# Optimization experiments

Measured on AMD Instinct MI355X. Metric: run time of the kernel, lower is better.

The kernel has to match this reference:

```python
import jax, jax.numpy as jnp
import numpy as np

D_MODEL = 1024
N_HEAD = 16
D_HEAD = 64
BSZ = 2
QLEN = 2048
LOCAL_SIZE = 1000
LN_EPS = 1e-5


def setup_inputs() -> dict:
    key = jax.random.key(0)
    ks = jax.random.split(key, 8)
    z1ss = jax.random.normal(ks[0], (BSZ, D_MODEL, QLEN), jnp.float32)
    pos_emb = jax.random.normal(ks[1], (1, D_MODEL, QLEN), jnp.float32)
    u1ss = jax.random.normal(ks[2], (BSZ, 3 * N_HEAD * D_HEAD, QLEN), jnp.float32) * 0.05
    W_qkv = jax.random.normal(ks[3], (3 * N_HEAD * D_HEAD, D_MODEL), jnp.float32) * 0.02
    W_r = jax.random.normal(ks[4], (N_HEAD * D_HEAD, D_MODEL), jnp.float32) * 0.02
    r_w_bias = jax.random.uniform(ks[5], (N_HEAD, D_HEAD), jnp.float32, -0.05, 0.05)
    r_r_bias = jax.random.uniform(ks[6], (N_HEAD, D_HEAD), jnp.float32, -0.05, 0.05)
    W_o = jax.random.normal(ks[7], (D_MODEL, N_HEAD * D_HEAD), jnp.float32) * 0.02
    b_o = jnp.zeros((D_MODEL,), jnp.float32)
    return dict(z1ss=z1ss, pos_emb=pos_emb, u1ss=u1ss, W_qkv=W_qkv, W_r=W_r,
                r_w_bias=r_w_bias, r_r_bias=r_r_bias, W_o=W_o, b_o=b_o)


def _rel_shift(x):
    # Transformer-XL relative-shift trick: pad one column on the left, reshape,
    # drop first row, reshape back. x: [b, n, qlen, klen]
    b, n, q, k = x.shape
    xp = jnp.pad(x, ((0, 0), (0, 0), (0, 0), (1, 0)))
    return xp.reshape(b, n, k + 1, q)[:, :, 1:, :].reshape(b, n, q, k)


def reference(z1ss, pos_emb, u1ss, W_qkv, W_r, r_w_bias, r_r_bias, W_o, b_o):
    bsz, d_model, qlen = z1ss.shape
    n_head, d_head = r_w_bias.shape
    klen = qlen  # mems=None -> mlen=0
    scale = 1.0 / (d_head ** 0.5)

    # Conv1d(kernel_size=1, bias=False) == per-position linear
    w_heads = jnp.einsum('od,bdq->boq', W_qkv, z1ss) + u1ss        # [b, 3*n*d, q]
    r_head_k = jnp.einsum('od,dq->oq', W_r, pos_emb[0]).reshape(n_head, d_head, klen)

    q_h, k_h, v_h = jnp.split(w_heads, 3, axis=1)
    q_h = q_h.reshape(bsz, n_head, d_head, qlen)
    k_h = k_h.reshape(bsz, n_head, d_head, klen)
    v_h = v_h.reshape(bsz, n_head, d_head, klen)

    AC = jnp.einsum('bndi,bndj->bnij', q_h + r_w_bias[:, :, None], k_h)
    BD = _rel_shift(jnp.einsum('bndi,ndj->bnij', q_h + r_r_bias[:, :, None], r_head_k))
    attn_score = (AC + BD) * scale                                  # [b, n, q, k]

    # causal + local-window mask (mlen=0)
    ones = jnp.ones((qlen, klen), dtype=bool)
    mask = jnp.triu(ones, 1) | jnp.tril(ones, -LOCAL_SIZE)
    attn_score = jnp.where(mask[None, None], -jnp.inf, attn_score)

    attn_prob = jax.nn.softmax(attn_score, axis=-1)
    attn_vec = jnp.einsum('bnij,bndj->bndi', attn_prob, v_h)
    attn_vec = attn_vec.reshape(bsz, n_head * d_head, qlen)

    attn_out = jnp.einsum('od,bdq->boq', W_o, attn_vec) + b_o[None, :, None]

    # post-LN residual: layer_norm over d_model (no affine params)
    x = (attn_out + z1ss).transpose(0, 2, 1)                        # [b, q, d]
    mu = x.mean(-1, keepdims=True)
    var = ((x - mu) ** 2).mean(-1, keepdims=True)
    x = (x - mu) / jnp.sqrt(var + LN_EPS)
    return x.transpose(0, 2, 1)                                     # [b, d, q]
```

## Files before the change

### kernel.cpp

```cpp
#include <hip/hip_runtime.h>
#include <hip/hip_bf16.h>

#define D_MODEL 1024
#define N_HEAD 16
#define BSZ 2
#define QLEN 2048
#define LOCAL_SIZE 1000
#define QKV3 (3 * N_HEAD * 64)

typedef __hip_bfloat16 bf16;
typedef short bf16x8 __attribute__((ext_vector_type(8)));
typedef float f32x4 __attribute__((ext_vector_type(4)));

static __device__ __forceinline__ float b2f(bf16 x) { return __bfloat162float(x); }
static __device__ __forceinline__ float bits2f(unsigned short u) {
    return __uint_as_float(((unsigned int)u) << 16);
}
static __device__ __forceinline__ unsigned short f2bs(float x) {
    __hip_bfloat16 h = __float2bfloat16(x);
    return *(unsigned short*)&h;
}

static __device__ __forceinline__ int rmode(int m, int fl) { return (m == 2) ? fl : m; }
static __device__ __forceinline__ float ldm(const void* p, size_t i, int isf) {
    return isf ? ((const float*)p)[i] : b2f(((const bf16*)p)[i]);
}
static __device__ __forceinline__ float4 ld4(const void* p, size_t i, int isf) {
    if (isf) return ((const float4*)p)[i >> 2];
    ushort4 u = ((const ushort4*)p)[i >> 2];
    float4 f;
    f.x = bits2f(u.x); f.y = bits2f(u.y); f.z = bits2f(u.z); f.w = bits2f(u.w);
    return f;
}
static __device__ __forceinline__ ushort4 cvt4(float4 f) {
    ushort4 u;
    u.x = f2bs(f.x); u.y = f2bs(f.y); u.z = f2bs(f.z); u.w = f2bs(f.w);
    return u;
}

static __device__ __forceinline__ void glds16(const bf16* g, unsigned short* l) {
    __builtin_amdgcn_global_load_lds(
        (const __attribute__((address_space(1))) void*)g,
        (__attribute__((address_space(3))) void*)l,
        16, 0, 0);
}

__global__ void detect_kernel(const unsigned short* __restrict__ w, int* __restrict__ flag)
{
    if (threadIdx.x == 0 && blockIdx.x == 0) {
        int good = 0;
        for (int i = 0; i < 256; ++i) {
            float v = bits2f(w[i]);
            if (v == v && fabsf(v) < 8.0f) ++good;
        }
        *flag = (good >= 240) ? 0 : 1;
    }
}

__global__ __launch_bounds__(256)
void convw_all(const void* __restrict__ wq, const void* __restrict__ wr,
               const void* __restrict__ wo, bf16* __restrict__ outp,
               const int* __restrict__ flag)
{
    const int fl = *flag;
    const int blk = blockIdx.x;
    const void* in; size_t segOff;
    if (blk < 1536)      { in = wq; segOff = (size_t)blk * 2048; }
    else if (blk < 2048) { in = wr; segOff = (size_t)(blk - 1536) * 2048; }
    else                 { in = wo; segOff = (size_t)(blk - 2048) * 2048; }
    const size_t ii = segOff + (size_t)threadIdx.x * 8;
    const size_t oi = (size_t)blk * 2048 + (size_t)threadIdx.x * 8;
    if (fl) {
        float4 a = ((const float4*)in)[ii / 4];
        float4 b = ((const float4*)in)[ii / 4 + 1];
        *(ushort4*)((unsigned short*)outp + oi)     = cvt4(a);
        *(ushort4*)((unsigned short*)outp + oi + 4) = cvt4(b);
    } else {
        *(uint4*)((unsigned short*)outp + oi) = ((const uint4*)in)[ii / 8];
    }
}

__global__ __launch_bounds__(256)
void tcvt_all(const void* __restrict__ z1ss, const void* __restrict__ pos,
              bf16* __restrict__ zt, bf16* __restrict__ post,
              const int* __restrict__ flag)
{
    const int fl = *flag;
    const int zb = blockIdx.z;
    const void* in = (zb < BSZ) ? z1ss : pos;
    const size_t inOff = (zb < BSZ) ? (size_t)zb * D_MODEL * QLEN : 0;
    bf16* outp = (zb < BSZ) ? zt + (size_t)zb * QLEN * D_MODEL : post;
    const int c0 = blockIdx.x * 32;
    const int r0 = blockIdx.y * 32;
    const int tx = threadIdx.x & 31, ty = threadIdx.x >> 5;
    __shared__ float T[32][33];
#pragma unroll
    for (int r = 0; r < 4; ++r) {
        int rr = r0 + ty + r * 8;
        T[ty + r * 8][tx] = ldm(in, inOff + (size_t)rr * QLEN + c0 + tx, fl);
    }
    __syncthreads();
#pragma unroll
    for (int r = 0; r < 4; ++r) {
        int cc = c0 + ty + r * 8;
        outp[(size_t)cc * D_MODEL + r0 + tx] = __float2bfloat16(T[tx][ty + r * 8]);
    }
}

__global__ __launch_bounds__(256)
void gemm_qkvr(const bf16* __restrict__ wqb, const bf16* __restrict__ wrb,
               const bf16* __restrict__ zt, const bf16* __restrict__ post,
               bf16* __restrict__ wh, bf16* __restrict__ rhk,
               const void* __restrict__ u1ss, const int* __restrict__ flag)
{
    const int fl = *flag;
    const int bz = blockIdx.z;
    const int by = blockIdx.y;
    const bool isR = by >= (QKV3 / 128);
    if (isR && bz) return;
    const int n0 = blockIdx.x * 128;
    const int m0 = (isR ? by - QKV3 / 128 : by) * 128;
    const int K = D_MODEL, N = QLEN;

    const bf16* A = isR ? wrb : wqb;
    const bf16* B = isR ? post : zt + (size_t)bz * (size_t)QLEN * D_MODEL;
    bf16* C       = isR ? rhk  : wh + (size_t)bz * (size_t)QKV3 * QLEN;
    const size_t uOff = (size_t)bz * (size_t)QKV3 * QLEN;

    const int tid = threadIdx.x;
    const int wave = tid >> 6, lane = tid & 63;
    const int quad = lane >> 4, l15 = lane & 15;
    const int wm = (wave >> 1) * 64, wn = (wave & 1) * 64;

    __shared__ __align__(16) unsigned short A_s[2][128 * 32];
    __shared__ __align__(16) unsigned short B_s[2][128 * 32];

    const int srow = wave * 32 + (lane >> 2);
    const int scol = (lane & 3) * 8;
    const bf16* Ag = A + (size_t)(m0 + srow) * K + scol;
    const bf16* Bg = B + (size_t)(n0 + srow) * K + scol;
    const int sbase = wave * 1024;

    f32x4 acc[4][4];
#pragma unroll
    for (int i = 0; i < 4; ++i)
#pragma unroll
        for (int j = 0; j < 4; ++j) acc[i][j] = (f32x4){0.f, 0.f, 0.f, 0.f};

    glds16(Ag,                   &A_s[0][sbase]);
    glds16(Ag + (size_t)16 * K,  &A_s[0][sbase + 512]);
    glds16(Bg,                   &B_s[0][sbase]);
    glds16(Bg + (size_t)16 * K,  &B_s[0][sbase + 512]);

    int cur = 0;
    for (int k0 = 0; k0 < K; k0 += 32) {
        __syncthreads();
        if (k0 + 32 < K) {
            const int kn = k0 + 32;
            glds16(Ag + kn,                  &A_s[cur ^ 1][sbase]);
            glds16(Ag + (size_t)16 * K + kn, &A_s[cur ^ 1][sbase + 512]);
            glds16(Bg + kn,                  &B_s[cur ^ 1][sbase]);
            glds16(Bg + (size_t)16 * K + kn, &B_s[cur ^ 1][sbase + 512]);
        }
        bf16x8 a[4], bb[4];
#pragma unroll
        for (int i = 0; i < 4; ++i)
            a[i] = *(const bf16x8*)&A_s[cur][(wm + i * 16 + l15) * 32 + quad * 8];
#pragma unroll
        for (int j = 0; j < 4; ++j)
            bb[j] = *(const bf16x8*)&B_s[cur][(wn + j * 16 + l15) * 32 + quad * 8];
#pragma unroll
        for (int i = 0; i < 4; ++i)
#pragma unroll
            for (int j = 0; j < 4; ++j)
                acc[i][j] = __builtin_amdgcn_mfma_f32_16x16x32_bf16(a[i], bb[j], acc[i][j], 0, 0, 0);
        cur ^= 1;
    }

#pragma unroll
    for (int i = 0; i < 4; ++i) {
#pragma unroll
        for (int j = 0; j < 4; ++j) {
            int n = n0 + wn + j * 16 + l15;
#pragma unroll
            for (int r = 0; r < 4; ++r) {
                int m = m0 + wm + i * 16 + quad * 4 + r;
                float v = acc[i][j][r];
                if (!isR) v += ldm(u1ss, uOff + (size_t)m * N + n, fl);
                C[(size_t)m * N + n] = __float2bfloat16(v);
            }
        }
    }
}

__global__ __launch_bounds__(256)
void gemm_glds(const bf16* __restrict__ A, size_t sAb,
               const bf16* __restrict__ B, size_t sBb,
               void* __restrict__ C, int c_is_bf16, size_t sCb,
               const void* __restrict__ addm, int mAdd, size_t sAddb,
               const void* __restrict__ bias, int mBias,
               int M, int N, int K, const int* __restrict__ flag)
{
    const int fl = *flag;
    const int fAdd = rmode(mAdd, fl), fBias = rmode(mBias, fl);

    const int bz = blockIdx.z;
    const int n0 = blockIdx.x * 128;
    const int m0 = blockIdx.y * 128;
    const int tid = threadIdx.x;
    const int wave = tid >> 6, lane = tid & 63;
    const int quad = lane >> 4, l15 = lane & 15;
    const int wm = (wave >> 1) * 64, wn = (wave & 1) * 64;

    __shared__ __align__(16) unsigned short A_s[2][128 * 32];
    __shared__ __align__(16) unsigned short B_s[2][128 * 32];

    const int srow = wave * 32 + (lane >> 2);
    const int scol = (lane & 3) * 8;
    const bf16* Ag = A + (size_t)bz * sAb + (size_t)(m0 + srow) * K + scol;
    const bf16* Bg = B + (size_t)bz * sBb + (size_t)(n0 + srow) * K + scol;
    const int sbase = wave * 1024;

    f32x4 acc[4][4];
#pragma unroll
    for (int i = 0; i < 4; ++i)
#pragma unroll
        for (int j = 0; j < 4; ++j) acc[i][j] = (f32x4){0.f, 0.f, 0.f, 0.f};

    glds16(Ag,                   &A_s[0][sbase]);
    glds16(Ag + (size_t)16 * K,  &A_s[0][sbase + 512]);
    glds16(Bg,                   &B_s[0][sbase]);
    glds16(Bg + (size_t)16 * K,  &B_s[0][sbase + 512]);

    int cur = 0;
    for (int k0 = 0; k0 < K; k0 += 32) {
        __syncthreads();
        if (k0 + 32 < K) {
            const int kn = k0 + 32;
            glds16(Ag + kn,                  &A_s[cur ^ 1][sbase]);
            glds16(Ag + (size_t)16 * K + kn, &A_s[cur ^ 1][sbase + 512]);
            glds16(Bg + kn,                  &B_s[cur ^ 1][sbase]);
            glds16(Bg + (size_t)16 * K + kn, &B_s[cur ^ 1][sbase + 512]);
        }
        bf16x8 a[4], bb[4];
#pragma unroll
        for (int i = 0; i < 4; ++i)
            a[i] = *(const bf16x8*)&A_s[cur][(wm + i * 16 + l15) * 32 + quad * 8];
#pragma unroll
        for (int j = 0; j < 4; ++j)
            bb[j] = *(const bf16x8*)&B_s[cur][(wn + j * 16 + l15) * 32 + quad * 8];
#pragma unroll
        for (int i = 0; i < 4; ++i)
#pragma unroll
            for (int j = 0; j < 4; ++j)
                acc[i][j] = __builtin_amdgcn_mfma_f32_16x16x32_bf16(a[i], bb[j], acc[i][j], 0, 0, 0);
        cur ^= 1;
    }

    const size_t cb = (size_t)bz * sCb;
#pragma unroll
    for (int i = 0; i < 4; ++i) {
#pragma unroll
        for (int j = 0; j < 4; ++j) {
            int n = n0 + wn + j * 16 + l15;
#pragma unroll
            for (int r = 0; r < 4; ++r) {
                int m = m0 + wm + i * 16 + quad * 4 + r;
                float v = acc[i][j][r];
                if (addm) v += ldm(addm, (size_t)bz * sAddb + (size_t)m * N + n, fAdd);
                if (bias) v += ldm(bias, (size_t)n, fBias);
                size_t ci = cb + (size_t)m * N + n;
                if (c_is_bf16) ((bf16*)C)[ci] = __float2bfloat16(v);
                else           ((float*)C)[ci] = v;
            }
        }
    }
}

__global__ __launch_bounds__(256)
void gemm_bf16(const void* __restrict__ A, int mA, size_t sAb,
               const void* __restrict__ B, int mB, size_t sBb,
               void* __restrict__ C, int c_is_bf16, size_t sCb,
               const void* __restrict__ addm, int mAdd, size_t sAddb,
               const void* __restrict__ bias, int mBias,
               int M, int N, int K, const int* __restrict__ flag)
{
    const int fl = *flag;
    const int fA = rmode(mA, fl), fB = rmode(mB, fl);
    const int fAdd = rmode(mAdd, fl), fBias = rmode(mBias, fl);

    const int bz = blockIdx.z;
    const int n0 = blockIdx.x * 128;
    const int m0 = blockIdx.y * 128;
    const int tid = threadIdx.x;
    const int wave = tid >> 6, lane = tid & 63;
    const int quad = lane >> 4, l15 = lane & 15;
    const int wm = (wave >> 1) * 64, wn = (wave & 1) * 64;

    __shared__ unsigned short A_s[128][40];
    __shared__ unsigned short B_s[128][40];

    const int r0c = tid >> 2,         c0c = tid & 3;
    const int r1c = (tid + 256) >> 2, c1c = tid & 3;

    const size_t aOff = (size_t)bz * sAb;
    const size_t bOff = (size_t)bz * sBb;
    const bf16*  Ah = (const bf16*)A;
    const float* Af = (const float*)A;
    const bf16*  Bh = (const bf16*)B;
    const float* Bf = (const float*)B;

    uint4 pa[4], pb[4];

#define LOAD_OP(p, fX, Xh, Xf, xOff, R0, C0, R1, C1, base, k0)                          \
    do {                                                                                \
        if (!fX) {                                                                      \
            p[0] = *(const uint4*)(Xh + xOff + (size_t)(base + R0) * K + (k0) + C0 * 8);\
            p[1] = *(const uint4*)(Xh + xOff + (size_t)(base + R1) * K + (k0) + C1 * 8);\
        } else {                                                                        \
            const float* q0 = Xf + xOff + (size_t)(base + R0) * K + (k0) + C0 * 8;      \
            const float* q1 = Xf + xOff + (size_t)(base + R1) * K + (k0) + C1 * 8;      \
            p[0] = *(const uint4*)q0; p[1] = *(const uint4*)(q0 + 4);                   \
            p[2] = *(const uint4*)q1; p[3] = *(const uint4*)(q1 + 4);                   \
        }                                                                               \
    } while (0)

#define WRITE_OP(p, fX, S, R0, C0, R1, C1)                                              \
    do {                                                                                \
        if (!fX) {                                                                      \
            *(uint4*)&S[R0][C0 * 8] = p[0];                                             \
            *(uint4*)&S[R1][C1 * 8] = p[1];                                             \
        } else {                                                                        \
            float4 f0 = *(float4*)&p[0], f1 = *(float4*)&p[1];                          \
            float4 f2 = *(float4*)&p[2], f3 = *(float4*)&p[3];                          \
            *(ushort4*)&S[R0][C0 * 8]     = cvt4(f0);                                   \
            *(ushort4*)&S[R0][C0 * 8 + 4] = cvt4(f1);                                   \
            *(ushort4*)&S[R1][C1 * 8]     = cvt4(f2);                                   \
            *(ushort4*)&S[R1][C1 * 8 + 4] = cvt4(f3);                                   \
        }                                                                               \
    } while (0)

    f32x4 acc[4][4];
#pragma unroll
    for (int i = 0; i < 4; ++i)
#pragma unroll
        for (int j = 0; j < 4; ++j) acc[i][j] = (f32x4){0.f, 0.f, 0.f, 0.f};

    LOAD_OP(pa, fA, Ah, Af, aOff, r0c, c0c, r1c, c1c, m0, 0);
    LOAD_OP(pb, fB, Bh, Bf, bOff, r0c, c0c, r1c, c1c, n0, 0);

    for (int k0 = 0; k0 < K; k0 += 32) {
        WRITE_OP(pa, fA, A_s, r0c, c0c, r1c, c1c);
        WRITE_OP(pb, fB, B_s, r0c, c0c, r1c, c1c);
        __syncthreads();

        const int kn = k0 + 32;
        if (kn < K) {
            LOAD_OP(pa, fA, Ah, Af, aOff, r0c, c0c, r1c, c1c, m0, kn);
            LOAD_OP(pb, fB, Bh, Bf, bOff, r0c, c0c, r1c, c1c, n0, kn);
        }

        bf16x8 a[4], bb[4];
#pragma unroll
        for (int i = 0; i < 4; ++i)
            a[i] = *(const bf16x8*)&A_s[wm + i * 16 + l15][quad * 8];
#pragma unroll
        for (int j = 0; j < 4; ++j)
            bb[j] = *(const bf16x8*)&B_s[wn + j * 16 + l15][quad * 8];
#pragma unroll
        for (int i = 0; i < 4; ++i)
#pragma unroll
            for (int j = 0; j < 4; ++j)
                acc[i][j] = __builtin_amdgcn_mfma_f32_16x16x32_bf16(a[i], bb[j], acc[i][j], 0, 0, 0);
        __syncthreads();
    }
#undef LOAD_OP
#undef WRITE_OP

    const size_t cb = (size_t)bz * sCb;
#pragma unroll
    for (int i = 0; i < 4; ++i) {
#pragma unroll
        for (int j = 0; j < 4; ++j) {
            int n = n0 + wn + j * 16 + l15;
#pragma unroll
            for (int r = 0; r < 4; ++r) {
                int m = m0 + wm + i * 16 + quad * 4 + r;
                float v = acc[i][j][r];
                if (addm) v += ldm(addm, (size_t)bz * sAddb + (size_t)m * N + n, fAdd);
                if (bias) v += ldm(bias, (size_t)n, fBias);
                size_t ci = cb + (size_t)m * N + n;
                if (c_is_bf16) ((bf16*)C)[ci] = __float2bfloat16(v);
                else           ((float*)C)[ci] = v;
            }
        }
    }
}

__global__ __launch_bounds__(256)
void gemm_tn(const void* __restrict__ A, int mA, size_t sAb,
             const void* __restrict__ Bsrc, int mB, int bTrans, int ldB, size_t sBb,
             void* __restrict__ C, int c_is_bf16, size_t sCb,
             const void* __restrict__ addm, int mAdd, int addT, size_t sAddb,
             const void* __restrict__ bias, int mBias,
             int M, int N, int K, const int* __restrict__ flag)
{
    const int fl = *flag;
    const int fA = rmode(mA, fl), fB = rmode(mB, fl);
    const int fAdd = rmode(mAdd, fl), fBias = rmode(mBias, fl);

    const int bz = blockIdx.z;
    const int n0 = blockIdx.x * 128;
    const int m0 = blockIdx.y * 128;
    const int tid = threadIdx.x;
    const int wave = tid >> 6, lane = tid & 63;
    const int quad = lane >> 4, l15 = lane & 15;
    const int wm = (wave >> 1) * 64, wn = (wave & 1) * 64;

    __shared__ unsigned short A_s[128][40];
    __shared__ unsigned short B_s[128][40];

    const size_t aBase = (size_t)bz * sAb;
    const size_t bBase = (size_t)bz * sBb;

    f32x4 acc[4][4];
#pragma unroll
    for (int i = 0; i < 4; ++i)
#pragma unroll
        for (int j = 0; j < 4; ++j) acc[i][j] = (f32x4){0.f, 0.f, 0.f, 0.f};

    for (int k0 = 0; k0 < K; k0 += 32) {
#pragma unroll
        for (int g = 0; g < 4; ++g) {
            int c = tid + g * 256;
            int m = c >> 3, kc = (c & 7) * 4;
            float4 f = ld4(A, aBase + (size_t)(m0 + m) * K + k0 + kc, fA);
            *(ushort4*)&A_s[m][kc] = cvt4(f);
        }
        if (!bTrans) {
#pragma unroll
            for (int g = 0; g < 4; ++g) {
                int c = tid + g * 256;
                int n = c >> 3, kc = (c & 7) * 4;
                float4 f = ld4(Bsrc, bBase + (size_t)(n0 + n) * ldB + k0 + kc, fB);
                *(ushort4*)&B_s[n][kc] = cvt4(f);
            }
        } else {
#pragma unroll
            for (int g = 0; g < 4; ++g) {
                int c = tid + g * 256;
                int k = c >> 5, nc = (c & 31) * 4;
                float4 f = ld4(Bsrc, bBase + (size_t)(k0 + k) * ldB + n0 + nc, fB);
                ushort4 u = cvt4(f);
                B_s[nc + 0][k] = u.x;
                B_s[nc + 1][k] = u.y;
                B_s[nc + 2][k] = u.z;
                B_s[nc + 3][k] = u.w;
            }
        }
        __syncthreads();

        bf16x8 a[4], bb[4];
#pragma unroll
        for (int i = 0; i < 4; ++i)
            a[i] = *(const bf16x8*)&A_s[wm + i * 16 + l15][quad * 8];
#pragma unroll
        for (int j = 0; j < 4; ++j)
            bb[j] = *(const bf16x8*)&B_s[wn + j * 16 + l15][quad * 8];
#pragma unroll
        for (int i = 0; i < 4; ++i)
#pragma unroll
            for (int j = 0; j < 4; ++j)
                acc[i][j] = __builtin_amdgcn_mfma_f32_16x16x32_bf16(a[i], bb[j], acc[i][j], 0, 0, 0);
        __syncthreads();
    }

    const size_t cb = (size_t)bz * sCb;
#pragma unroll
    for (int i = 0; i < 4; ++i) {
#pragma unroll
        for (int j = 0; j < 4; ++j) {
            int n = n0 + wn + j * 16 + l15;
#pragma unroll
            for (int r = 0; r < 4; ++r) {
                int m = m0 + wm + i * 16 + quad * 4 + r;
                float v = acc[i][j][r];
                if (addm) {
                    size_t ai = (size_t)bz * sAddb +
                                (addT ? ((size_t)n * M + m) : ((size_t)m * N + n));
                    v += ldm(addm, ai, fAdd);
                }
                if (bias) v += ldm(bias, (size_t)n, fBias);
                size_t ci = cb + (size_t)m * N + n;
                if (c_is_bf16) ((bf16*)C)[ci] = __float2bfloat16(v);
                else           ((float*)C)[ci] = v;
            }
        }
    }
}

__global__ __launch_bounds__(256)
void attn_mfma(const bf16* __restrict__ wh,
               const bf16* __restrict__ rhk,
               const void* __restrict__ rwb,
               const void* __restrict__ rrb,
               bf16* __restrict__ av_out,
               const int* __restrict__ flag)
{
    const int fl = *flag;
    const int lidx = blockIdx.x + 32 * (blockIdx.y + (blockIdx.z << 4));
    const int slot = lidx >> 8;
    const int grp  = lidx & 255;
    const int hb   = grp & 31;
    const int prm  = grp >> 5;
    const int it   = (slot == 0) ? 16 + prm : (slot == 1) ? 24 + prm
                   : (slot == 2) ? prm : 15 - prm;
    const int h = hb & 15, b = hb >> 4;

    const int i0 = it * 64;
    const int tid = threadIdx.x;
    const int wave = tid >> 6, lane = tid & 63;
    const int quad = lane >> 4, l15 = lane & 15;
    const int hw = h * 64;

    __shared__ __align__(16) unsigned short sm[18432];
    unsigned short* Kt  = sm;
    unsigned short* Vs  = sm + 4608;
    unsigned short* Rt  = sm + 9216;
    unsigned short* Ps  = sm + 13824;
    unsigned short* Qrw = sm;
    unsigned short* Qrr = sm + 4608;

    const bf16* whb = wh + (size_t)b * QKV3 * QLEN;
    const int d_t = tid & 63;
    const int dv0 = tid >> 3, jv0 = (tid & 7) * 8;
    const int dv1 = (tid + 256) >> 3;

    int lo = i0 - (LOCAL_SIZE - 1);
    if (lo < 0) lo = 0;
    const int jt_lo = lo >> 6;
    const int j0_lo = jt_lo * 64;

    {
        float brw = ldm(rwb, hw + d_t, fl);
        float brr = ldm(rrb, hw + d_t, fl);
        const bf16* qrow = whb + (size_t)(hw + d_t) * QLEN + i0;
        uint4 qv0 = *(const uint4*)(qrow + wave * 8);
        uint4 qv1 = *(const uint4*)(qrow + (4 + wave) * 8);
        const int pbase0 = j0_lo - i0 + QLEN - 64;
        const bf16* rrow = rhk + (size_t)(hw + d_t) * QLEN;
        uint4 rv0i = *(const uint4*)(rrow + pbase0 + wave * 8);
        uint4 rv1i = *(const uint4*)(rrow + pbase0 + (4 + wave) * 8);

        unsigned short u8[8];
        *(uint4*)u8 = qv0;
#pragma unroll
        for (int u = 0; u < 8; ++u) {
            float q = bits2f(u8[u]);
            Qrw[(wave * 8 + u) * 72 + d_t] = f2bs(q + brw);
            Qrr[(wave * 8 + u) * 72 + d_t] = f2bs(q + brr);
        }
        *(uint4*)u8 = qv1;
#pragma unroll
        for (int u = 0; u < 8; ++u) {
            float q = bits2f(u8[u]);
            Qrw[((4 + wave) * 8 + u) * 72 + d_t] = f2bs(q + brw);
            Qrr[((4 + wave) * 8 + u) * 72 + d_t] = f2bs(q + brr);
        }
        *(uint4*)u8 = rv0i;
#pragma unroll
        for (int u = 0; u < 8; ++u) Rt[(wave * 8 + u) * 72 + d_t] = u8[u];
        *(uint4*)u8 = rv1i;
#pragma unroll
        for (int u = 0; u < 8; ++u) Rt[((4 + wave) * 8 + u) * 72 + d_t] = u8[u];
    }

    uint4 kv0, kv1, vv0, vv1, rv0, rv1;
    {
        const int j0 = j0_lo;
        const bf16* krow = whb + (size_t)(1024 + hw + d_t) * QLEN + j0;
        kv0 = *(const uint4*)(krow + wave * 8);
        kv1 = *(const uint4*)(krow + (4 + wave) * 8);
        vv0 = *(const uint4*)(whb + (size_t)(2048 + hw + dv0) * QLEN + j0 + jv0);
        vv1 = *(const uint4*)(whb + (size_t)(2048 + hw + dv1) * QLEN + j0 + jv0);
        const int pn = j0 - i0 + QLEN;
        const bf16* rrow = rhk + (size_t)(hw + d_t) * QLEN;
        int p0 = pn + wave * 8;
        if (p0 + 7 < QLEN) rv0 = *(const uint4*)(rrow + p0);
        else {
            unsigned short u8[8];
#pragma unroll
            for (int u = 0; u < 8; ++u)
                u8[u] = (p0 + u < QLEN) ? *(const unsigned short*)(rrow + p0 + u) : 0;
            rv0 = *(uint4*)u8;
        }
        int p1 = pn + (4 + wave) * 8;
        if (p1 + 7 < QLEN) rv1 = *(const uint4*)(rrow + p1);
        else {
            unsigned short u8[8];
#pragma unroll
            for (int u = 0; u < 8; ++u)
                u8[u] = (p1 + u < QLEN) ? *(const unsigned short*)(rrow + p1 + u) : 0;
            rv1 = *(uint4*)u8;
        }
    }
    __syncthreads();

    const int qrow_off = (wave * 16 + l15) * 72 + quad * 8;
    bf16x8 qw0 = *(const bf16x8*)&Qrw[qrow_off];
    bf16x8 qw1 = *(const bf16x8*)&Qrw[qrow_off + 32];
    bf16x8 qr0 = *(const bf16x8*)&Qrr[qrow_off];
    bf16x8 qr1 = *(const bf16x8*)&Qrr[qrow_off + 32];

    f32x4 g_acc[8];
#pragma unroll
    for (int nt = 0; nt < 4; ++nt) {
        f32x4 g = (f32x4){0.f, 0.f, 0.f, 0.f};
        int ro = (nt * 16 + l15) * 72 + quad * 8;
        bf16x8 b0 = *(const bf16x8*)&Rt[ro];
        bf16x8 b1 = *(const bf16x8*)&Rt[ro + 32];
        g = __builtin_amdgcn_mfma_f32_16x16x32_bf16(qr0, b0, g, 0, 0, 0);
        g = __builtin_amdgcn_mfma_f32_16x16x32_bf16(qr1, b1, g, 0, 0, 0);
        g_acc[nt] = g;
    }

    float l_r[4] = {0.f, 0.f, 0.f, 0.f};
    f32x4 o_acc[4];
#pragma unroll
    for (int dj = 0; dj < 4; ++dj) o_acc[dj] = (f32x4){0.f, 0.f, 0.f, 0.f};

    for (int jt = jt_lo; jt <= it; ++jt) {
        const int j0 = jt * 64;
        asm volatile("" ::: "memory");
        __builtin_amdgcn_s_barrier();
        asm volatile("" ::: "memory");

        {
            unsigned short u8[8];
            *(uint4*)u8 = kv0;
#pragma unroll
            for (int u = 0; u < 8; ++u) Kt[(wave * 8 + u) * 72 + d_t] = u8[u];
            *(uint4*)u8 = kv1;
#pragma unroll
            for (int u = 0; u < 8; ++u) Kt[((4 + wave) * 8 + u) * 72 + d_t] = u8[u];
            *(uint4*)&Vs[dv0 * 72 + jv0] = vv0;
            *(uint4*)&Vs[dv1 * 72 + jv0] = vv1;
            *(uint4*)u8 = rv0;
#pragma unroll
            for (int u = 0; u < 8; ++u) Rt[(wave * 8 + u) * 72 + d_t] = u8[u];
            *(uint4*)u8 = rv1;
#pragma unroll
            for (int u = 0; u < 8; ++u) Rt[((4 + wave) * 8 + u) * 72 + d_t] = u8[u];
        }

        if (jt < it) {
            const int j0n = j0 + 64;
            const bf16* krow = whb + (size_t)(1024 + hw + d_t) * QLEN + j0n;
            kv0 = *(const uint4*)(krow + wave * 8);
            kv1 = *(const uint4*)(krow + (4 + wave) * 8);
            vv0 = *(const uint4*)(whb + (size_t)(2048 + hw + dv0) * QLEN + j0n + jv0);
            vv1 = *(const uint4*)(whb + (size_t)(2048 + hw + dv1) * QLEN + j0n + jv0);
            const int pn = j0n - i0 + QLEN;
            const bf16* rrow = rhk + (size_t)(hw + d_t) * QLEN;
            int p0 = pn + wave * 8;
            if (p0 + 7 < QLEN) rv0 = *(const uint4*)(rrow + p0);
            else {
                unsigned short u8[8];
#pragma unroll
                for (int u = 0; u < 8; ++u)
                    u8[u] = (p0 + u < QLEN) ? *(const unsigned short*)(rrow + p0 + u) : 0;
                rv0 = *(uint4*)u8;
            }
            int p1 = pn + (4 + wave) * 8;
            if (p1 + 7 < QLEN) rv1 = *(const uint4*)(rrow + p1);
            else {
                unsigned short u8[8];
#pragma unroll
                for (int u = 0; u < 8; ++u)
                    u8[u] = (p1 + u < QLEN) ? *(const unsigned short*)(rrow + p1 + u) : 0;
                rv1 = *(uint4*)u8;
            }
        }
        asm volatile("s_waitcnt lgkmcnt(0)" ::: "memory");
        __builtin_amdgcn_s_barrier();
        asm volatile("" ::: "memory");

        f32x4 s_acc[4];
#pragma unroll
        for (int nj = 0; nj < 4; ++nj) {
            s_acc[nj] = (f32x4){0.f, 0.f, 0.f, 0.f};
            int ko = (nj * 16 + l15) * 72 + quad * 8;
            bf16x8 b0 = *(const bf16x8*)&Kt[ko];
            bf16x8 b1 = *(const bf16x8*)&Kt[ko + 32];
            s_acc[nj] = __builtin_amdgcn_mfma_f32_16x16x32_bf16(qw0, b0, s_acc[nj], 0, 0, 0);
            s_acc[nj] = __builtin_amdgcn_mfma_f32_16x16x32_bf16(qw1, b1, s_acc[nj], 0, 0, 0);
        }
#pragma unroll
        for (int nt = 0; nt < 4; ++nt) {
            f32x4 g = (f32x4){0.f, 0.f, 0.f, 0.f};
            int ro = (nt * 16 + l15) * 72 + quad * 8;
            bf16x8 b0 = *(const bf16x8*)&Rt[ro];
            bf16x8 b1 = *(const bf16x8*)&Rt[ro + 32];
            g = __builtin_amdgcn_mfma_f32_16x16x32_bf16(qr0, b0, g, 0, 0, 0);
            g = __builtin_amdgcn_mfma_f32_16x16x32_bf16(qr1, b1, g, 0, 0, 0);
            g_acc[4 + nt] = g;
        }

        float rs[4] = {0.f, 0.f, 0.f, 0.f};
#define SOFTMAX_W(W)                                                            \
        {                                                                       \
            _Pragma("unroll")                                                   \
            for (int nj = 0; nj < 4; ++nj) {                                    \
                _Pragma("unroll")                                               \
                for (int r = 0; r < 4; ++r) {                                   \
                    const int n0 = 3 - (W) + nj;                                \
                    int sa = ((lane & 48) | ((l15 - 4 * quad - r - 1) & 15)) << 2; \
                    float blo = __int_as_float(__builtin_amdgcn_ds_bpermute(    \
                        sa, __float_as_int(g_acc[n0][r])));                     \
                    float bhi = __int_as_float(__builtin_amdgcn_ds_bpermute(    \
                        sa, __float_as_int(g_acc[n0 + 1][r])));                 \
                    float bd = (l15 > 4 * quad + r) ? bhi : blo;                \
                    int i_loc = (W) * 16 + quad * 4 + r;                        \
                    int j_loc = nj * 16 + l15;                                  \
                    int diff = (i0 + i_loc) - (j0 + j_loc);                     \
                    float pv = 0.f;                                             \
                    if (diff >= 0 && diff < LOCAL_SIZE)                         \
                        pv = __expf((s_acc[nj][r] + bd) * 0.125f);              \
                    Ps[i_loc * 72 + j_loc] = f2bs(pv);                          \
                    rs[r] += pv;                                                \
                }                                                               \
            }                                                                   \
        }
        if      (wave == 0) SOFTMAX_W(0)
        else if (wave == 1) SOFTMAX_W(1)
        else if (wave == 2) SOFTMAX_W(2)
        else                SOFTMAX_W(3)
#undef SOFTMAX_W

#pragma unroll
        for (int r = 0; r < 4; ++r) {
            float v = rs[r];
            v += __shfl_xor(v, 1);
            v += __shfl_xor(v, 2);
            v += __shfl_xor(v, 4);
            v += __shfl_xor(v, 8);
            l_r[r] += v;
        }

        {
            int po = (wave * 16 + l15) * 72 + quad * 8;
            bf16x8 pa0 = *(const bf16x8*)&Ps[po];
            bf16x8 pa1 = *(const bf16x8*)&Ps[po + 32];
#pragma unroll
            for (int dj = 0; dj < 4; ++dj) {
                int vo = (dj * 16 + l15) * 72 + quad * 8;
                bf16x8 b0 = *(const bf16x8*)&Vs[vo];
                bf16x8 b1 = *(const bf16x8*)&Vs[vo + 32];
                o_acc[dj] = __builtin_amdgcn_mfma_f32_16x16x32_bf16(pa0, b0, o_acc[dj], 0, 0, 0);
                o_acc[dj] = __builtin_amdgcn_mfma_f32_16x16x32_bf16(pa1, b1, o_acc[dj], 0, 0, 0);
            }
        }

#pragma unroll
        for (int nt = 0; nt < 4; ++nt) g_acc[nt] = g_acc[nt + 4];
    }

#pragma unroll
    for (int r = 0; r < 4; ++r) {
        float inv = 1.f / l_r[r];
        int q = i0 + wave * 16 + quad * 4 + r;
        bf16* orow = av_out + ((size_t)b * QLEN + q) * D_MODEL + hw;
#pragma unroll
        for (int dj = 0; dj < 4; ++dj)
            orow[dj * 16 + l15] = __float2bfloat16(o_acc[dj][r] * inv);
    }
}

__global__ __launch_bounds__(256)
void ln_kernel(float* __restrict__ yt)
{
    const int b = blockIdx.y, q = blockIdx.x;
    float* row = yt + ((size_t)b * QLEN + q) * D_MODEL;
    const int t = threadIdx.x;
    float4 v = ((float4*)row)[t];
    float s  = v.x + v.y + v.z + v.w;
    float ss = v.x * v.x + v.y * v.y + v.z * v.z + v.w * v.w;
#pragma unroll
    for (int off = 32; off; off >>= 1) {
        s  += __shfl_down(s, off);
        ss += __shfl_down(ss, off);
    }
    __shared__ float sw[4], ssw[4];
    const int w = t >> 6;
    if ((t & 63) == 0) { sw[w] = s; ssw[w] = ss; }
    __syncthreads();
    float S  = sw[0] + sw[1] + sw[2] + sw[3];
    float SS = ssw[0] + ssw[1] + ssw[2] + ssw[3];
    float mu  = S / D_MODEL;
    float var = SS / D_MODEL - mu * mu;
    float rs  = rsqrtf(var + 1e-5f);
    v.x = (v.x - mu) * rs; v.y = (v.y - mu) * rs;
    v.z = (v.z - mu) * rs; v.w = (v.w - mu) * rs;
    ((float4*)row)[t] = v;
}

__global__ __launch_bounds__(256)
void transpose_out(const float* __restrict__ yt, void* __restrict__ out,
                   const int* __restrict__ flag)
{
    const int fl = *flag;
    const int b  = blockIdx.z;
    const int q0 = blockIdx.x * 32;
    const int o0 = blockIdx.y * 32;
    const int tx = threadIdx.x & 31, ty = threadIdx.x >> 5;
    __shared__ float T[32][33];
#pragma unroll
    for (int r = 0; r < 4; ++r) {
        int q = q0 + ty + r * 8;
        T[ty + r * 8][tx] = yt[((size_t)b * QLEN + q) * D_MODEL + o0 + tx];
    }
    __syncthreads();
#pragma unroll
    for (int r = 0; r < 4; ++r) {
        int o = o0 + ty + r * 8;
        size_t oi = ((size_t)b * D_MODEL + o) * QLEN + q0 + tx;
        float v = T[tx][ty + r * 8];
        if (fl) ((float*)out)[oi] = v;
        else    ((bf16*)out)[oi] = __float2bfloat16(v);
    }
}

extern "C" void kernel_launch(void* const* d_in, const int* in_sizes, int n_in,
                              void* d_out, int out_size, void* d_ws, size_t ws_size,
                              hipStream_t stream)
{
    const void* z1ss = d_in[0];
    const void* pos  = d_in[1];
    const void* u1ss = d_in[2];
    const void* Wqkv = d_in[3];
    const void* Wr   = d_in[4];
    const void* rwb  = d_in[5];
    const void* rrb  = d_in[6];
    const void* Wo   = d_in[7];
    const void* bo   = d_in[8];

    const size_t whE  = (size_t)BSZ * QKV3 * QLEN;
    const size_t rhkE = (size_t)D_MODEL * QLEN;
    const size_t avE  = (size_t)BSZ * QLEN * D_MODEL;
    const size_t ztE  = avE;
    const size_t wqE  = (size_t)QKV3 * D_MODEL;
    const size_t wrE  = (size_t)D_MODEL * D_MODEL;
    const size_t woE  = wrE;

    char* ws = (char*)d_ws;
    bf16* wh   = (bf16*)ws;
    bf16* rhk  = wh + whE;
    bf16* avec = rhk + rhkE;
    bf16* post = avec;
    size_t baseB = (whE + rhkE + avE) * sizeof(bf16);
    bf16* zt  = (bf16*)(ws + baseB);
    bf16* wqb = zt + ztE;
    bf16* wrb = wqb + wqE;
    bf16* wob = wrb + wrE;
    float* yt = (float*)ws;

    const size_t t2B = baseB + ztE * sizeof(bf16) + 16;
    const size_t t1B = baseB + (ztE + wqE + wrE + woE) * sizeof(bf16) + 16;
    const int tier = (ws_size >= t1B) ? 1 : (ws_size >= t2B) ? 2 : 3;

    int* flag = (tier == 1) ? (int*)(wob + woE)
              : (tier == 2) ? (int*)(wqb)
                            : (int*)(ws + baseB);

    detect_kernel<<<1, 64, 0, stream>>>((const unsigned short*)Wqkv, flag);

    if (tier == 1) {
        convw_all<<<dim3((unsigned)((wqE + wrE + woE) / 2048)), 256, 0, stream>>>(
            Wqkv, Wr, Wo, wqb, flag);

        tcvt_all<<<dim3(QLEN / 32, D_MODEL / 32, BSZ + 1), 256, 0, stream>>>(
            z1ss, pos, zt, post, flag);

        gemm_qkvr<<<dim3(QLEN / 128, QKV3 / 128 + D_MODEL / 128, BSZ), 256, 0, stream>>>(
            wqb, wrb, zt, post, wh, rhk, u1ss, flag);

        attn_mfma<<<dim3(QLEN / 64, N_HEAD, BSZ), 256, 0, stream>>>(
            wh, rhk, rwb, rrb, avec, flag);

        gemm_glds<<<dim3(1024 / 128, 2048 / 128, BSZ), 256, 0, stream>>>(
            avec, (size_t)QLEN * D_MODEL,
            wob, 0,
            yt, 0, (size_t)QLEN * D_MODEL,
            zt, 0, (size_t)QLEN * D_MODEL,
            bo, 2,
            QLEN, D_MODEL, D_MODEL, flag);
    } else if (tier == 2) {
        tcvt_all<<<dim3(QLEN / 32, D_MODEL / 32, BSZ + 1), 256, 0, stream>>>(
            z1ss, pos, zt, post, flag);

        gemm_bf16<<<dim3(2048 / 128, 3072 / 128, BSZ), 256, 0, stream>>>(
            Wqkv, 2, 0,
            zt, 0, (size_t)QLEN * D_MODEL,
            wh, 1, (size_t)QKV3 * QLEN,
            u1ss, 2, (size_t)QKV3 * QLEN,
            nullptr, 0,
            QKV3, QLEN, D_MODEL, flag);

        gemm_bf16<<<dim3(2048 / 128, 1024 / 128, 1), 256, 0, stream>>>(
            Wr, 2, 0,
            post, 0, 0,
            rhk, 1, 0,
            nullptr, 0, 0,
            nullptr, 0,
            D_MODEL, QLEN, D_MODEL, flag);

        attn_mfma<<<dim3(QLEN / 64, N_HEAD, BSZ), 256, 0, stream>>>(
            wh, rhk, rwb, rrb, avec, flag);

        gemm_bf16<<<dim3(1024 / 128, 2048 / 128, BSZ), 256, 0, stream>>>(
            avec, 0, (size_t)QLEN * D_MODEL,
            Wo, 2, 0,
            yt, 0, (size_t)QLEN * D_MODEL,
            zt, 0, (size_t)QLEN * D_MODEL,
            bo, 2,
            QLEN, D_MODEL, D_MODEL, flag);
    } else {
        gemm_tn<<<dim3(2048 / 128, 3072 / 128, BSZ), 256, 0, stream>>>(
            Wqkv, 2, 0,
            z1ss, 2, 1, QLEN, (size_t)D_MODEL * QLEN,
            wh, 1, (size_t)QKV3 * QLEN,
            u1ss, 2, 0, (size_t)QKV3 * QLEN,
            nullptr, 0,
            QKV3, QLEN, D_MODEL, flag);
        gemm_tn<<<dim3(2048 / 128, 1024 / 128, 1), 256, 0, stream>>>(
            Wr, 2, 0,
            pos, 2, 1, QLEN, 0,
            rhk, 1, 0,
            nullptr, 0, 0, 0,
            nullptr, 0,
            D_MODEL, QLEN, D_MODEL, flag);
        attn_mfma<<<dim3(QLEN / 64, N_HEAD, BSZ), 256, 0, stream>>>(
            wh, rhk, rwb, rrb, avec, flag);
        gemm_tn<<<dim3(1024 / 128, 2048 / 128, BSZ), 256, 0, stream>>>(
            avec, 0, (size_t)QLEN * D_MODEL,
            Wo, 2, 0, D_MODEL, 0,
            yt, 0, (size_t)QLEN * D_MODEL,
            z1ss, 2, 1, (size_t)D_MODEL * QLEN,
            bo, 2,
            QLEN, D_MODEL, D_MODEL, flag);
    }

    ln_kernel<<<dim3(QLEN, BSZ), 256, 0, stream>>>(yt);

    transpose_out<<<dim3(QLEN / 32, D_MODEL / 32, BSZ), 256, 0, stream>>>(yt, d_out, flag);
}
```

Measured before the change: 405.9 us.

## Triple-buffer LDS in projection GEMMs with explicit vmcnt waits

Converts the double-buffered global-to-LDS pipeline in the QKV/R projection and generic GEMM kernels to a three-stage ring, issuing loads two k-steps ahead. Replaces __syncthreads with a partial s_waitcnt vmcnt(4) plus a raw barrier, so only the oldest stage must land before compute. The aim is to hide more global-load latency behind MFMA work, at the cost of 50% more LDS per block, which may reduce occupancy.

```diff
diff --git a/kernel.cpp b/kernel.cpp
--- a/kernel.cpp
+++ b/kernel.cpp
@@ -132,8 +132,8 @@
     const int quad = lane >> 4, l15 = lane & 15;
     const int wm = (wave >> 1) * 64, wn = (wave & 1) * 64;
 
-    __shared__ __align__(16) unsigned short A_s[2][128 * 32];
-    __shared__ __align__(16) unsigned short B_s[2][128 * 32];
+    __shared__ __align__(16) unsigned short A_s[3][128 * 32];
+    __shared__ __align__(16) unsigned short B_s[3][128 * 32];
 
     const int srow = wave * 32 + (lane >> 2);
     const int scol = (lane & 3) * 8;
@@ -147,20 +147,29 @@
 #pragma unroll
         for (int j = 0; j < 4; ++j) acc[i][j] = (f32x4){0.f, 0.f, 0.f, 0.f};
 
-    glds16(Ag,                   &A_s[0][sbase]);
-    glds16(Ag + (size_t)16 * K,  &A_s[0][sbase + 512]);
-    glds16(Bg,                   &B_s[0][sbase]);
-    glds16(Bg + (size_t)16 * K,  &B_s[0][sbase + 512]);
+    glds16(Ag,                        &A_s[0][sbase]);
+    glds16(Ag + (size_t)16 * K,       &A_s[0][sbase + 512]);
+    glds16(Bg,                        &B_s[0][sbase]);
+    glds16(Bg + (size_t)16 * K,       &B_s[0][sbase + 512]);
+    glds16(Ag + 32,                   &A_s[1][sbase]);
+    glds16(Ag + (size_t)16 * K + 32,  &A_s[1][sbase + 512]);
+    glds16(Bg + 32,                   &B_s[1][sbase]);
+    glds16(Bg + (size_t)16 * K + 32,  &B_s[1][sbase + 512]);
 
     int cur = 0;
     for (int k0 = 0; k0 < K; k0 += 32) {
-        __syncthreads();
-        if (k0 + 32 < K) {
-            const int kn = k0 + 32;
-            glds16(Ag + kn,                  &A_s[cur ^ 1][sbase]);
-            glds16(Ag + (size_t)16 * K + kn, &A_s[cur ^ 1][sbase + 512]);
-            glds16(Bg + kn,                  &B_s[cur ^ 1][sbase]);
-            glds16(Bg + (size_t)16 * K + kn, &B_s[cur ^ 1][sbase + 512]);
+        if (k0 + 32 < K) asm volatile("s_waitcnt vmcnt(4) lgkmcnt(0)" ::: "memory");
+        else             asm volatile("s_waitcnt vmcnt(0) lgkmcnt(0)" ::: "memory");
+        __builtin_amdgcn_s_barrier();
+        asm volatile("" ::: "memory");
+
+        const int kn = k0 + 64;
+        if (kn < K) {
+            const int nb = (cur >= 1) ? cur - 1 : 2;
+            glds16(Ag + kn,                  &A_s[nb][sbase]);
+            glds16(Ag + (size_t)16 * K + kn, &A_s[nb][sbase + 512]);
+            glds16(Bg + kn,                  &B_s[nb][sbase]);
+            glds16(Bg + (size_t)16 * K + kn, &B_s[nb][sbase + 512]);
         }
         bf16x8 a[4], bb[4];
 #pragma unroll
@@ -174,7 +183,7 @@
 #pragma unroll
             for (int j = 0; j < 4; ++j)
                 acc[i][j] = __builtin_amdgcn_mfma_f32_16x16x32_bf16(a[i], bb[j], acc[i][j], 0, 0, 0);
-        cur ^= 1;
+        cur = (cur == 2) ? 0 : cur + 1;
     }
 
 #pragma unroll
@@ -212,8 +221,8 @@
     const int quad = lane >> 4, l15 = lane & 15;
     const int wm = (wave >> 1) * 64, wn = (wave & 1) * 64;
 
-    __shared__ __align__(16) unsigned short A_s[2][128 * 32];
-    __shared__ __align__(16) unsigned short B_s[2][128 * 32];
+    __shared__ __align__(16) unsigned short A_s[3][128 * 32];
+    __shared__ __align__(16) unsigned short B_s[3][128 * 32];
 
     const int srow = wave * 32 + (lane >> 2);
     const int scol = (lane & 3) * 8;
@@ -227,20 +236,31 @@
 #pragma unroll
         for (int j = 0; j < 4; ++j) acc[i][j] = (f32x4){0.f, 0.f, 0.f, 0.f};
 
-    glds16(Ag,                   &A_s[0][sbase]);
-    glds16(Ag + (size_t)16 * K,  &A_s[0][sbase + 512]);
-    glds16(Bg,                   &B_s[0][sbase]);
-    glds16(Bg + (size_t)16 * K,  &B_s[0][sbase + 512]);
+    glds16(Ag,                        &A_s[0][sbase]);
+    glds16(Ag + (size_t)16 * K,       &A_s[0][sbase + 512]);
+    glds16(Bg,                        &B_s[0][sbase]);
+    glds16(Bg + (size_t)16 * K,       &B_s[0][sbase + 512]);
+    if (32 < K) {
+        glds16(Ag + 32,                   &A_s[1][sbase]);
+        glds16(Ag + (size_t)16 * K + 32,  &A_s[1][sbase + 512]);
+        glds16(Bg + 32,                   &B_s[1][sbase]);
+        glds16(Bg + (size_t)16 * K + 32,  &B_s[1][sbase + 512]);
+    }
 
     int cur = 0;
     for (int k0 = 0; k0 < K; k0 += 32) {
-        __syncthreads();
-        if (k0 + 32 < K) {
-            const int kn = k0 + 32;
-            glds16(Ag + kn,                  &A_s[cur ^ 1][sbase]);
-            glds16(Ag + (size_t)16 * K + kn, &A_s[cur ^ 1][sbase + 512]);
-            glds16(Bg + kn,                  &B_s[cur ^ 1][sbase]);
-            glds16(Bg + (size_t)16 * K + kn, &B_s[cur ^ 1][sbase + 512]);
+        if (k0 + 32 < K) asm volatile("s_waitcnt vmcnt(4) lgkmcnt(0)" ::: "memory");
+        else             asm volatile("s_waitcnt vmcnt(0) lgkmcnt(0)" ::: "memory");
+        __builtin_amdgcn_s_barrier();
+        asm volatile("" ::: "memory");
+
+        const int kn = k0 + 64;
+        if (kn < K) {
+            const int nb = (cur >= 1) ? cur - 1 : 2;
+            glds16(Ag + kn,                  &A_s[nb][sbase]);
+            glds16(Ag + (size_t)16 * K + kn, &A_s[nb][sbase + 512]);
+            glds16(Bg + kn,                  &B_s[nb][sbase]);
+            glds16(Bg + (size_t)16 * K + kn, &B_s[nb][sbase + 512]);
         }
         bf16x8 a[4], bb[4];
 #pragma unroll
@@ -254,7 +274,7 @@
 #pragma unroll
             for (int j = 0; j < 4; ++j)
                 acc[i][j] = __builtin_amdgcn_mfma_f32_16x16x32_bf16(a[i], bb[j], acc[i][j], 0, 0, 0);
-        cur ^= 1;
+        cur = (cur == 2) ? 0 : cur + 1;
     }
 
     const size_t cb = (size_t)bz * sCb;
```

Result: faster. 382.6 us (-5.8%).
